# Performance work log

Hardware: AMD Instinct MI355X
Metric: run time of the kernel (lower is better)

## Reference

```python
import jax, jax.numpy as jnp
import numpy as np

N_NODES = 50000
N_EDGES = 800000
D = 64        # node feature dim (and edge feature dim, and msg output dim)
H_MSG = 256   # msg MLP hidden
H_UPD = 256   # upd MLP hidden


def setup_inputs() -> dict:
    key = jax.random.key(0)
    ks = jax.random.split(key, 12)
    h = jax.random.normal(ks[0], (N_NODES, D), dtype=jnp.float32)
    e = jax.random.normal(ks[1], (N_EDGES, D), dtype=jnp.float32)
    senders = jax.random.randint(ks[2], (N_EDGES,), 0, N_NODES, dtype=jnp.int32)
    receivers = jax.random.randint(ks[3], (N_EDGES,), 0, N_NODES, dtype=jnp.int32)
    d_msg_in = D + 2 * D   # concat([e, hs, hr])
    d_upd_in = 2 * D       # concat([h, agg])
    sc = lambda fan_in: 1.0 / np.sqrt(fan_in)
    W_m1 = jax.random.normal(ks[4], (d_msg_in, H_MSG), dtype=jnp.float32) * sc(d_msg_in)
    b_m1 = jnp.zeros((H_MSG,), dtype=jnp.float32)
    W_m2 = jax.random.normal(ks[5], (H_MSG, D), dtype=jnp.float32) * sc(H_MSG)
    b_m2 = jnp.zeros((D,), dtype=jnp.float32)
    W_u1 = jax.random.normal(ks[6], (d_upd_in, H_UPD), dtype=jnp.float32) * sc(d_upd_in)
    b_u1 = jnp.zeros((H_UPD,), dtype=jnp.float32)
    W_u2 = jax.random.normal(ks[7], (H_UPD, D), dtype=jnp.float32) * sc(H_UPD)
    b_u2 = jnp.zeros((D,), dtype=jnp.float32)
    return {
        "h": h, "e": e, "senders": senders, "receivers": receivers,
        "W_m1": W_m1, "b_m1": b_m1, "W_m2": W_m2, "b_m2": b_m2,
        "W_u1": W_u1, "b_u1": b_u1, "W_u2": W_u2, "b_u2": b_u2,
    }


def reference(h, e, senders, receivers, W_m1, b_m1, W_m2, b_m2, W_u1, b_u1, W_u2, b_u2):
    # message phase: gather endpoints, concat, 2-layer MLP
    hs = h[senders]                                   # [E, D]
    hr = h[receivers]                                 # [E, D]
    m_in = jnp.concatenate([e, hs, hr], axis=-1)      # [E, 3D]
    m = jax.nn.relu(m_in @ W_m1 + b_m1) @ W_m2 + b_m2 # [E, D]
    # aggregate messages at receivers
    agg = jax.ops.segment_sum(m, receivers, num_segments=h.shape[0])  # [N, D]
    # node update MLP + residual
    u_in = jnp.concatenate([h, agg], axis=-1)         # [N, 2D]
    dh = jax.nn.relu(u_in @ W_u1 + b_u1) @ W_u2 + b_u2
    return h + dh
```

## Files before the change

kernel.cpp:

```cpp
#include <hip/hip_runtime.h>
#include <hip/hip_bf16.h>
#include <cstdint>
#include <cstddef>

#define NNODES 50000
#define NEDGES 800000
#define DF 64
#define KM 192
#define KU 128
#define SROW 264

typedef __bf16 bf16_t;
typedef __bf16 bf16x8 __attribute__((ext_vector_type(8)));
typedef __bf16 bf16x4 __attribute__((ext_vector_type(4)));
typedef float  f32x4  __attribute__((ext_vector_type(4)));

__global__ void prep_kernel(const float* __restrict__ Wm1, const float* __restrict__ Wm2,
                            const float* __restrict__ Wu1, const float* __restrict__ Wu2,
                            bf16_t* __restrict__ wp)
{
    int idx = blockIdx.x * 256 + threadIdx.x;
    const float* src; int N; int off; int local;
    if (idx < 49152)       { src = Wm1; N = 256; off = 0;     local = idx; }
    else if (idx < 65536)  { src = Wm2; N = 64;  off = 49152; local = idx - 49152; }
    else if (idx < 98304)  { src = Wu1; N = 256; off = 65536; local = idx - 65536; }
    else if (idx < 114688) { src = Wu2; N = 64;  off = 98304; local = idx - 98304; }
    else return;
    int j    = local & 7;
    int l    = (local >> 3) & 63;
    int frag = local >> 9;
    int nct  = N >> 4;
    int kblk = frag / nct;
    int ct   = frag - kblk * nct;
    int k = kblk * 32 + (l >> 4) * 8 + j;
    int n = ct * 16 + (l & 15);
    wp[off + local] = (bf16_t)src[(size_t)k * N + n];
}

__device__ __forceinline__ void st_bf16x4(bf16_t* p, float4 v) {
    bf16x4 bv;
    bv[0] = (bf16_t)v.x; bv[1] = (bf16_t)v.y; bv[2] = (bf16_t)v.z; bv[3] = (bf16_t)v.w;
    *reinterpret_cast<bf16x4*>(p) = bv;
}

__global__ __launch_bounds__(512, 4)
void msg_kernel(const float* __restrict__ h, const float* __restrict__ efeat,
                const int* __restrict__ snd, const int* __restrict__ rcv,
                const bf16_t* __restrict__ Wp1, const float* __restrict__ b1,
                const bf16_t* __restrict__ Wp2, const float* __restrict__ b2,
                float* __restrict__ agg)
{
    __shared__ bf16_t s_buf[128 * SROW];
    __shared__ int s_snd[128];
    __shared__ int s_rcv[128];

    const int t  = threadIdx.x;
    const int e0 = blockIdx.x * 128;

    if (t < 128)      s_snd[t]       = snd[e0 + t];
    else if (t < 256) s_rcv[t - 128] = rcv[e0 + t - 128];
    __syncthreads();

    #pragma unroll
    for (int it = 0; it < 4; ++it) {
        int i = t + it * 512; int row = i >> 4; int col = (i & 15) * 4;
        float4 v = *reinterpret_cast<const float4*>(efeat + (size_t)(e0 + row) * DF + col);
        st_bf16x4(&s_buf[row * SROW + col], v);
    }
    #pragma unroll
    for (int it = 0; it < 4; ++it) {
        int i = t + it * 512; int row = i >> 4; int col = (i & 15) * 4;
        float4 v = *reinterpret_cast<const float4*>(h + (size_t)s_snd[row] * DF + col);
        st_bf16x4(&s_buf[row * SROW + DF + col], v);
    }
    #pragma unroll
    for (int it = 0; it < 4; ++it) {
        int i = t + it * 512; int row = i >> 4; int col = (i & 15) * 4;
        float4 v = *reinterpret_cast<const float4*>(h + (size_t)s_rcv[row] * DF + col);
        st_bf16x4(&s_buf[row * SROW + 2 * DF + col], v);
    }
    __syncthreads();

    const int w = t >> 6;
    const int l = t & 63;
    const int q = l >> 4;
    const int r = l & 15;

    f32x4 acc[2][8];
    #pragma unroll
    for (int g = 0; g < 2; ++g)
        #pragma unroll
        for (int am = 0; am < 8; ++am) acc[g][am] = (f32x4){0.f, 0.f, 0.f, 0.f};

    #pragma unroll
    for (int kb = 0; kb < 6; ++kb) {
        bf16x8 b0 = *reinterpret_cast<const bf16x8*>(Wp1 + ((size_t)(kb * 16 + w * 2 + 0) * 64 + l) * 8);
        bf16x8 b1f = *reinterpret_cast<const bf16x8*>(Wp1 + ((size_t)(kb * 16 + w * 2 + 1) * 64 + l) * 8);
        #pragma unroll
        for (int am = 0; am < 8; ++am) {
            bf16x8 a = *reinterpret_cast<const bf16x8*>(&s_buf[(am * 16 + r) * SROW + kb * 32 + q * 8]);
            acc[0][am] = __builtin_amdgcn_mfma_f32_16x16x32_bf16(a, b0,  acc[0][am], 0, 0, 0);
            acc[1][am] = __builtin_amdgcn_mfma_f32_16x16x32_bf16(a, b1f, acc[1][am], 0, 0, 0);
        }
    }
    __syncthreads();

    #pragma unroll
    for (int g = 0; g < 2; ++g) {
        int col = (w * 2 + g) * 16 + r;
        float bias = b1[col];
        #pragma unroll
        for (int am = 0; am < 8; ++am)
            #pragma unroll
            for (int j = 0; j < 4; ++j)
                s_buf[(am * 16 + q * 4 + j) * SROW + col] =
                    (bf16_t)fmaxf(acc[g][am][j] + bias, 0.f);
    }
    __syncthreads();

    const int m2  = w >> 2;
    const int ct2 = w & 3;
    f32x4 acc2[4];
    #pragma unroll
    for (int am = 0; am < 4; ++am) acc2[am] = (f32x4){0.f, 0.f, 0.f, 0.f};

    #pragma unroll
    for (int kb = 0; kb < 8; ++kb) {
        bf16x8 b = *reinterpret_cast<const bf16x8*>(Wp2 + ((size_t)(kb * 4 + ct2) * 64 + l) * 8);
        #pragma unroll
        for (int am = 0; am < 4; ++am) {
            bf16x8 a = *reinterpret_cast<const bf16x8*>(&s_buf[(m2 * 64 + am * 16 + r) * SROW + kb * 32 + q * 8]);
            acc2[am] = __builtin_amdgcn_mfma_f32_16x16x32_bf16(a, b, acc2[am], 0, 0, 0);
        }
    }

    float bias2 = b2[ct2 * 16 + r];
    #pragma unroll
    for (int am = 0; am < 4; ++am)
        #pragma unroll
        for (int j = 0; j < 4; ++j) {
            int erow = m2 * 64 + am * 16 + q * 4 + j;
            atomicAdd(agg + (size_t)s_rcv[erow] * DF + ct2 * 16 + r, acc2[am][j] + bias2);
        }
}

__global__ __launch_bounds__(256, 4)
void upd_kernel(const float* __restrict__ h, const float* __restrict__ agg,
                const bf16_t* __restrict__ Wp1, const float* __restrict__ b1,
                const bf16_t* __restrict__ Wp2, const float* __restrict__ b2,
                float* __restrict__ out)
{
    __shared__ bf16_t s_buf[64 * SROW];

    const int t  = threadIdx.x;
    const int n0 = blockIdx.x * 64;

    #pragma unroll
    for (int it = 0; it < 8; ++it) {
        int i    = t + it * 256;
        int nn   = i >> 5;
        int col  = (i & 31) * 4;
        int node = n0 + nn;
        float4 v;
        if (node < NNODES) {
            const float* srcp = (col < DF) ? (h + (size_t)node * DF + col)
                                           : (agg + (size_t)node * DF + (col - DF));
            v = *reinterpret_cast<const float4*>(srcp);
        } else {
            v.x = 0.f; v.y = 0.f; v.z = 0.f; v.w = 0.f;
        }
        st_bf16x4(&s_buf[nn * SROW + col], v);
    }
    __syncthreads();

    const int w = t >> 6;
    const int l = t & 63;
    const int q = l >> 4;
    const int r = l & 15;

    f32x4 acc[4][4];
    #pragma unroll
    for (int g = 0; g < 4; ++g)
        #pragma unroll
        for (int am = 0; am < 4; ++am) acc[g][am] = (f32x4){0.f, 0.f, 0.f, 0.f};

    #pragma unroll
    for (int kb = 0; kb < 4; ++kb) {
        bf16x8 a[4];
        #pragma unroll
        for (int am = 0; am < 4; ++am)
            a[am] = *reinterpret_cast<const bf16x8*>(&s_buf[(am * 16 + r) * SROW + kb * 32 + q * 8]);
        #pragma unroll
        for (int g = 0; g < 4; ++g) {
            int ct = w * 4 + g;
            bf16x8 b = *reinterpret_cast<const bf16x8*>(Wp1 + ((size_t)(kb * 16 + ct) * 64 + l) * 8);
            #pragma unroll
            for (int am = 0; am < 4; ++am)
                acc[g][am] = __builtin_amdgcn_mfma_f32_16x16x32_bf16(a[am], b, acc[g][am], 0, 0, 0);
        }
    }
    __syncthreads();

    #pragma unroll
    for (int g = 0; g < 4; ++g) {
        int col = (w * 4 + g) * 16 + r;
        float bias = b1[col];
        #pragma unroll
        for (int am = 0; am < 4; ++am)
            #pragma unroll
            for (int j = 0; j < 4; ++j)
                s_buf[(am * 16 + q * 4 + j) * SROW + col] =
                    (bf16_t)fmaxf(acc[g][am][j] + bias, 0.f);
    }
    __syncthreads();

    f32x4 acc2[4];
    #pragma unroll
    for (int am = 0; am < 4; ++am) acc2[am] = (f32x4){0.f, 0.f, 0.f, 0.f};

    #pragma unroll
    for (int kb = 0; kb < 8; ++kb) {
        bf16x8 a[4];
        #pragma unroll
        for (int am = 0; am < 4; ++am)
            a[am] = *reinterpret_cast<const bf16x8*>(&s_buf[(am * 16 + r) * SROW + kb * 32 + q * 8]);
        bf16x8 b = *reinterpret_cast<const bf16x8*>(Wp2 + ((size_t)(kb * 4 + w) * 64 + l) * 8);
        #pragma unroll
        for (int am = 0; am < 4; ++am)
            acc2[am] = __builtin_amdgcn_mfma_f32_16x16x32_bf16(a[am], b, acc2[am], 0, 0, 0);
    }

    float bias2 = b2[w * 16 + r];
    #pragma unroll
    for (int am = 0; am < 4; ++am)
        #pragma unroll
        for (int j = 0; j < 4; ++j) {
            int node = n0 + am * 16 + q * 4 + j;
            if (node < NNODES) {
                int col = w * 16 + r;
                out[(size_t)node * DF + col] =
                    h[(size_t)node * DF + col] + acc2[am][j] + bias2;
            }
        }
}

extern "C" void kernel_launch(void* const* d_in, const int* in_sizes, int n_in,
                              void* d_out, int out_size, void* d_ws, size_t ws_size,
                              hipStream_t stream)
{
    const float* h    = (const float*)d_in[0];
    const float* e    = (const float*)d_in[1];
    const int*   snd  = (const int*)d_in[2];
    const int*   rcv  = (const int*)d_in[3];
    const float* W_m1 = (const float*)d_in[4];
    const float* b_m1 = (const float*)d_in[5];
    const float* W_m2 = (const float*)d_in[6];
    const float* b_m2 = (const float*)d_in[7];
    const float* W_u1 = (const float*)d_in[8];
    const float* b_u1 = (const float*)d_in[9];
    const float* W_u2 = (const float*)d_in[10];
    const float* b_u2 = (const float*)d_in[11];
    float* out = (float*)d_out;

    const size_t agg_bytes = (size_t)NNODES * DF * sizeof(float);
    const size_t wp_bytes  = 114688 * sizeof(bf16_t);

    float*  agg;
    bf16_t* wp;
    if (ws_size >= agg_bytes + wp_bytes) {
        agg = (float*)d_ws;
        wp  = (bf16_t*)((char*)d_ws + agg_bytes);
    } else {
        agg = out;
        wp  = (bf16_t*)d_ws;
    }

    bf16_t* Wp_m1 = wp;
    bf16_t* Wp_m2 = wp + 49152;
    bf16_t* Wp_u1 = wp + 65536;
    bf16_t* Wp_u2 = wp + 98304;

    prep_kernel<<<448, 256, 0, stream>>>(W_m1, W_m2, W_u1, W_u2, wp);
    hipMemsetAsync(agg, 0, agg_bytes, stream);

    msg_kernel<<<NEDGES / 128, 512, 0, stream>>>(h, e, snd, rcv,
                                                 Wp_m1, b_m1, Wp_m2, b_m2, agg);
    upd_kernel<<<(NNODES + 63) / 64, 256, 0, stream>>>(h, agg,
                                                       Wp_u1, b_u1, Wp_u2, b_u2, out);
}
```

Before: 231.3 us.

## Accumulate edge messages with packed fp16x2 atomics into half-precision aggregate buffer

Switches the scatter-add of edge messages from scalar fp32 atomics to packed v2f16 global atomics, using lane shuffles to pair adjacent columns, and stores the aggregate buffer in fp16. This halves the atomic count and the aggregate memory footprint, including the memset and the update kernel's read. It also moves a barrier so the index loads overlap with the edge-feature staging. It trades accumulation precision: summing roughly 16 messages per node in fp16 can add rounding error and risks overflow.

```diff
diff --git a/kernel.cpp b/kernel.cpp
--- a/kernel.cpp
+++ b/kernel.cpp
@@ -1,5 +1,6 @@
 #include <hip/hip_runtime.h>
 #include <hip/hip_bf16.h>
+#include <hip/hip_fp16.h>
 #include <cstdint>
 #include <cstddef>
 
@@ -14,6 +15,7 @@
 typedef __bf16 bf16x8 __attribute__((ext_vector_type(8)));
 typedef __bf16 bf16x4 __attribute__((ext_vector_type(4)));
 typedef float  f32x4  __attribute__((ext_vector_type(4)));
+typedef _Float16 f16x2 __attribute__((ext_vector_type(2)));
 
 __global__ void prep_kernel(const float* __restrict__ Wm1, const float* __restrict__ Wm2,
                             const float* __restrict__ Wu1, const float* __restrict__ Wu2,
@@ -43,12 +45,13 @@
     *reinterpret_cast<bf16x4*>(p) = bv;
 }
 
+template<bool H2>
 __global__ __launch_bounds__(512, 4)
 void msg_kernel(const float* __restrict__ h, const float* __restrict__ efeat,
                 const int* __restrict__ snd, const int* __restrict__ rcv,
                 const bf16_t* __restrict__ Wp1, const float* __restrict__ b1,
                 const bf16_t* __restrict__ Wp2, const float* __restrict__ b2,
-                float* __restrict__ agg)
+                void* __restrict__ aggv)
 {
     __shared__ bf16_t s_buf[128 * SROW];
     __shared__ int s_snd[128];
@@ -59,7 +62,6 @@
 
     if (t < 128)      s_snd[t]       = snd[e0 + t];
     else if (t < 256) s_rcv[t - 128] = rcv[e0 + t - 128];
-    __syncthreads();
 
     #pragma unroll
     for (int it = 0; it < 4; ++it) {
@@ -67,6 +69,8 @@
         float4 v = *reinterpret_cast<const float4*>(efeat + (size_t)(e0 + row) * DF + col);
         st_bf16x4(&s_buf[row * SROW + col], v);
     }
+    __syncthreads();
+
     #pragma unroll
     for (int it = 0; it < 4; ++it) {
         int i = t + it * 512; int row = i >> 4; int col = (i & 15) * 4;
@@ -107,14 +111,14 @@
 
     #pragma unroll
     for (int g = 0; g < 2; ++g) {
-        int col = (w * 2 + g) * 16 + r;
-        float bias = b1[col];
+        const int col1 = (w * 2 + g) * 16 + r;
+        const float bias1 = b1[col1];
         #pragma unroll
         for (int am = 0; am < 8; ++am)
             #pragma unroll
             for (int j = 0; j < 4; ++j)
-                s_buf[(am * 16 + q * 4 + j) * SROW + col] =
-                    (bf16_t)fmaxf(acc[g][am][j] + bias, 0.f);
+                s_buf[(am * 16 + q * 4 + j) * SROW + col1] =
+                    (bf16_t)fmaxf(acc[g][am][j] + bias1, 0.f);
     }
     __syncthreads();
 
@@ -134,18 +138,43 @@
         }
     }
 
-    float bias2 = b2[ct2 * 16 + r];
-    #pragma unroll
-    for (int am = 0; am < 4; ++am)
-        #pragma unroll
-        for (int j = 0; j < 4; ++j) {
-            int erow = m2 * 64 + am * 16 + q * 4 + j;
-            atomicAdd(agg + (size_t)s_rcv[erow] * DF + ct2 * 16 + r, acc2[am][j] + bias2);
-        }
-}
-
+    if constexpr (H2) {
+        _Float16* aggh = (_Float16*)aggv;
+        const int  cp  = ct2 * 16 + (r & ~1);
+        const bool odd = (r & 1);
+        const float blo = b2[cp], bhi = b2[cp + 1];
+        #pragma unroll
+        for (int am = 0; am < 4; ++am) {
+            float v0 = acc2[am][0], v1 = acc2[am][1], v2 = acc2[am][2], v3 = acc2[am][3];
+            float p0 = __shfl_xor(v0, 1), p1 = __shfl_xor(v1, 1);
+            float p2 = __shfl_xor(v2, 1), p3 = __shfl_xor(v3, 1);
+            float loA = odd ? p2 : v0, hiA = odd ? v2 : p0;
+            float loB = odd ? p3 : v1, hiB = odd ? v3 : p1;
+            int jbase = odd ? 2 : 0;
+            int erowA = m2 * 64 + am * 16 + q * 4 + jbase;
+            f16x2 hA = { (_Float16)(loA + blo), (_Float16)(hiA + bhi) };
+            f16x2 hB = { (_Float16)(loB + blo), (_Float16)(hiB + bhi) };
+            __builtin_amdgcn_global_atomic_fadd_v2f16(
+                (f16x2*)(aggh + (size_t)s_rcv[erowA]     * DF + cp), hA);
+            __builtin_amdgcn_global_atomic_fadd_v2f16(
+                (f16x2*)(aggh + (size_t)s_rcv[erowA + 1] * DF + cp), hB);
+        }
+    } else {
+        float* agg = (float*)aggv;
+        const float bias2 = b2[ct2 * 16 + r];
+        #pragma unroll
+        for (int am = 0; am < 4; ++am)
+            #pragma unroll
+            for (int j = 0; j < 4; ++j) {
+                int erow = m2 * 64 + am * 16 + q * 4 + j;
+                atomicAdd(agg + (size_t)s_rcv[erow] * DF + ct2 * 16 + r, acc2[am][j] + bias2);
+            }
+    }
+}
+
+template<bool H2>
 __global__ __launch_bounds__(256, 4)
-void upd_kernel(const float* __restrict__ h, const float* __restrict__ agg,
+void upd_kernel(const float* __restrict__ h, const void* __restrict__ aggv,
                 const bf16_t* __restrict__ Wp1, const float* __restrict__ b1,
                 const bf16_t* __restrict__ Wp2, const float* __restrict__ b2,
                 float* __restrict__ out)
@@ -155,21 +184,43 @@
     const int t  = threadIdx.x;
     const int n0 = blockIdx.x * 64;
 
-    #pragma unroll
-    for (int it = 0; it < 8; ++it) {
-        int i    = t + it * 256;
-        int nn   = i >> 5;
-        int col  = (i & 31) * 4;
-        int node = n0 + nn;
-        float4 v;
-        if (node < NNODES) {
-            const float* srcp = (col < DF) ? (h + (size_t)node * DF + col)
-                                           : (agg + (size_t)node * DF + (col - DF));
-            v = *reinterpret_cast<const float4*>(srcp);
-        } else {
-            v.x = 0.f; v.y = 0.f; v.z = 0.f; v.w = 0.f;
-        }
-        st_bf16x4(&s_buf[nn * SROW + col], v);
+    if constexpr (H2) {
+        const _Float16* aggh = (const _Float16*)aggv;
+        #pragma unroll
+        for (int it = 0; it < 4; ++it) {
+            int i = t + it * 256; int nn = i >> 4; int col = (i & 15) * 4;
+            int node = n0 + nn;
+            float4 v = {0.f, 0.f, 0.f, 0.f};
+            if (node < NNODES) v = *reinterpret_cast<const float4*>(h + (size_t)node * DF + col);
+            st_bf16x4(&s_buf[nn * SROW + col], v);
+        }
+        #pragma unroll
+        for (int it = 0; it < 4; ++it) {
+            int i = t + it * 256; int nn = i >> 4; int col = (i & 15) * 4;
+            int node = n0 + nn;
+            float4 v = {0.f, 0.f, 0.f, 0.f};
+            if (node < NNODES) {
+                f16x2 h01 = *reinterpret_cast<const f16x2*>(aggh + (size_t)node * DF + col);
+                f16x2 h23 = *reinterpret_cast<const f16x2*>(aggh + (size_t)node * DF + col + 2);
+                v.x = (float)h01[0]; v.y = (float)h01[1];
+                v.z = (float)h23[0]; v.w = (float)h23[1];
+            }
+            st_bf16x4(&s_buf[nn * SROW + DF + col], v);
+        }
+    } else {
+        const float* agg = (const float*)aggv;
+        #pragma unroll
+        for (int it = 0; it < 8; ++it) {
+            int i = t + it * 256; int nn = i >> 5; int col = (i & 31) * 4;
+            int node = n0 + nn;
+            float4 v = {0.f, 0.f, 0.f, 0.f};
+            if (node < NNODES) {
+                const float* srcp = (col < DF) ? (h + (size_t)node * DF + col)
+                                               : (agg + (size_t)node * DF + (col - DF));
+                v = *reinterpret_cast<const float4*>(srcp);
+            }
+            st_bf16x4(&s_buf[nn * SROW + col], v);
+        }
     }
     __syncthreads();
 
@@ -262,17 +313,22 @@
     const float* b_u2 = (const float*)d_in[11];
     float* out = (float*)d_out;
 
-    const size_t agg_bytes = (size_t)NNODES * DF * sizeof(float);
-    const size_t wp_bytes  = 114688 * sizeof(bf16_t);
-
-    float*  agg;
+    const size_t aggh_bytes = (size_t)NNODES * DF * sizeof(_Float16);
+    const size_t wp_bytes   = 114688 * sizeof(bf16_t);
+
+    const bool useH2 = (ws_size >= aggh_bytes + wp_bytes);
+
+    void*   aggv;
     bf16_t* wp;
-    if (ws_size >= agg_bytes + wp_bytes) {
-        agg = (float*)d_ws;
-        wp  = (bf16_t*)((char*)d_ws + agg_bytes);
+    size_t  agg_clear;
+    if (useH2) {
+        aggv = d_ws;
+        wp   = (bf16_t*)((char*)d_ws + aggh_bytes);
+        agg_clear = aggh_bytes;
     } else {
-        agg = out;
-        wp  = (bf16_t*)d_ws;
+        aggv = out;
+        wp   = (bf16_t*)d_ws;
+        agg_clear = (size_t)NNODES * DF * sizeof(float);
     }
 
     bf16_t* Wp_m1 = wp;
@@ -281,10 +337,17 @@
     bf16_t* Wp_u2 = wp + 98304;
 
     prep_kernel<<<448, 256, 0, stream>>>(W_m1, W_m2, W_u1, W_u2, wp);
-    hipMemsetAsync(agg, 0, agg_bytes, stream);
-
-    msg_kernel<<<NEDGES / 128, 512, 0, stream>>>(h, e, snd, rcv,
-                                                 Wp_m1, b_m1, Wp_m2, b_m2, agg);
-    upd_kernel<<<(NNODES + 63) / 64, 256, 0, stream>>>(h, agg,
-                                                       Wp_u1, b_u1, Wp_u2, b_u2, out);
-}
+    (void)hipMemsetAsync(aggv, 0, agg_clear, stream);
+
+    if (useH2) {
+        msg_kernel<true><<<NEDGES / 128, 512, 0, stream>>>(h, e, snd, rcv,
+                                                           Wp_m1, b_m1, Wp_m2, b_m2, aggv);
+        upd_kernel<true><<<(NNODES + 63) / 64, 256, 0, stream>>>(h, aggv,
+                                                                 Wp_u1, b_u1, Wp_u2, b_u2, out);
+    } else {
+        msg_kernel<false><<<NEDGES / 128, 512, 0, stream>>>(h, e, snd, rcv,
+                                                            Wp_m1, b_m1, Wp_m2, b_m2, aggv);
+        upd_kernel<false><<<(NNODES + 63) / 64, 256, 0, stream>>>(h, aggv,
+                                                                  Wp_u1, b_u1, Wp_u2, b_u2, out);
+    }
+}
```

After: 234.6 us. About the same (+1.4%).
